# Kernel tuning notes

Hardware: AMD Instinct MI355X
Metric: run time of the kernel (lower is better)

The kernel has to match this reference:

```python
import jax, jax.numpy as jnp
import numpy as np
import math

B, T, C, H = 4, 2048, 1024, 16
EPS = 1e-10

def setup_inputs() -> dict:
    key = jax.random.key(0)
    ks = jax.random.split(key, 9)
    s = 0.02
    return {
        "x": jax.random.normal(ks[0], (B, T, C), jnp.float32),
        "w_attn": jax.random.normal(ks[1], (3 * C, C), jnp.float32) * s,
        "b_attn": jax.random.normal(ks[2], (3 * C,), jnp.float32) * s,
        "w_proj": jax.random.normal(ks[3], (C, C), jnp.float32) * s,
        "b_proj": jax.random.normal(ks[4], (C,), jnp.float32) * s,
        "w_fc": jax.random.normal(ks[5], (4 * C, C), jnp.float32) * s,
        "b_fc": jax.random.normal(ks[6], (4 * C,), jnp.float32) * s,
        "w_mlp_proj": jax.random.normal(ks[7], (C, 4 * C), jnp.float32) * s,
        "b_mlp_proj": jax.random.normal(ks[8], (C,), jnp.float32) * s,
    }

def layernorm(x):
    # custom LayerNormalization: no gamma/beta, eps=1e-10, biased variance
    mean = jnp.mean(x, axis=-1, keepdims=True)
    xmu = x - mean
    var = jnp.mean(xmu * xmu, axis=-1, keepdims=True)
    return xmu / jnp.sqrt(var + EPS)

def new_gelu(x):
    # 0.5*x*(1+tanh(sqrt(2/pi)*(x+0.044715*x^3)))
    c = math.sqrt(2.0 / math.pi)
    return 0.5 * x * (1.0 + jnp.tanh(c * (x + 0.044715 * x * x * x)))

def attention(x, w_attn, b_attn, w_proj, b_proj):
    b, t, cdim = x.shape
    d = cdim // H
    ca = x @ w_attn.T + b_attn                      # [B,T,3C]
    q, k, v = jnp.split(ca, 3, axis=2)
    q = q.reshape(b, t, H, d)
    k = k.reshape(b, t, H, d)
    v = v.reshape(b, t, H, d)
    att = jnp.einsum('bthd,bshd->bhts', q, k) * (1.0 / math.sqrt(d))
    mask = jnp.tril(jnp.ones((t, t), dtype=bool))
    att = jnp.where(mask, att, -jnp.inf)
    att = jax.nn.softmax(att, axis=-1)
    y = jnp.einsum('bhts,bshd->bthd', att, v).reshape(b, t, cdim)
    return y @ w_proj.T + b_proj

def reference(x, w_attn, b_attn, w_proj, b_proj, w_fc, b_fc, w_mlp_proj, b_mlp_proj):
    x = x + attention(layernorm(x), w_attn, b_attn, w_proj, b_proj)
    h = new_gelu(layernorm(x) @ w_fc.T + b_fc)
    x = x + (h @ w_mlp_proj.T + b_mlp_proj)
    return x
```

## Files before the change

kernel.cpp:

```cpp
#include <hip/hip_runtime.h>
#include <math.h>

constexpr int Bb = 4;
constexpr int Tt = 2048;
constexpr int Cc = 1024;
constexpr int Hh = 16;
constexpr int Dh = 64;
constexpr int Mm = Bb * Tt;

typedef __attribute__((ext_vector_type(8))) short s16x8;
typedef __attribute__((ext_vector_type(4))) short s16x4;
typedef __attribute__((ext_vector_type(4))) float f32x4;

__device__ __forceinline__ unsigned short f2bf(float x) {
    unsigned u = __float_as_uint(x);
    u += 0x7FFFu + ((u >> 16) & 1u);
    return (unsigned short)(u >> 16);
}
__device__ __forceinline__ float bf2f(unsigned short h) {
    return __uint_as_float((unsigned)h << 16);
}

__device__ __forceinline__ void gld16(const void* g, void* l) {
    __builtin_amdgcn_global_load_lds(
        (const __attribute__((address_space(1))) void*)g,
        (__attribute__((address_space(3))) void*)l, 16, 0, 0);
}


__global__ __launch_bounds__(256) void ln_conv_kernel(const float* __restrict__ in,
                                                      char* __restrict__ out) {
    const int row = blockIdx.x;
    const float4 v = reinterpret_cast<const float4*>(in + (size_t)row * Cc)[threadIdx.x];
    float s = v.x + v.y + v.z + v.w;
    float q = v.x * v.x + v.y * v.y + v.z * v.z + v.w * v.w;
#pragma unroll
    for (int off = 32; off > 0; off >>= 1) {
        s += __shfl_xor(s, off);
        q += __shfl_xor(q, off);
    }
    __shared__ float red[2][4];
    const int wid = threadIdx.x >> 6;
    if ((threadIdx.x & 63) == 0) { red[0][wid] = s; red[1][wid] = q; }
    __syncthreads();
    s = red[0][0] + red[0][1] + red[0][2] + red[0][3];
    q = red[1][0] + red[1][1] + red[1][2] + red[1][3];
    const float mean = s * (1.0f / Cc);
    const float var = q * (1.0f / Cc) - mean * mean;
    const float rstd = rsqrtf(var + 1e-10f);
    float o[4] = {(v.x - mean) * rstd, (v.y - mean) * rstd,
                  (v.z - mean) * rstd, (v.w - mean) * rstd};
    s16x4 hv, lv;
#pragma unroll
    for (int j = 0; j < 4; ++j) {
        unsigned short h = f2bf(o[j]);
        hv[j] = (short)h;
        lv[j] = (short)f2bf(o[j] - bf2f(h));
    }
    const int c0 = threadIdx.x * 4;
    char* p = out + (size_t)row * 4096 + ((c0 >> 5) * 8 + ((c0 >> 3) & 3)) * 16 + (c0 & 7) * 2;
    *reinterpret_cast<s16x4*>(p) = hv;
    *reinterpret_cast<s16x4*>(p + 64) = lv;
}

__global__ __launch_bounds__(256) void wconv_kernel(const float* __restrict__ W,
                                                    char* __restrict__ out,
                                                    int noct, int oshift, int ldk) {
    const int idx = blockIdx.x * 256 + threadIdx.x;
    if (idx >= noct) return;
    const int r = idx >> oshift;
    const int oct = idx & ((1 << oshift) - 1);
    const float* p = W + (size_t)r * ldk + oct * 8;
    float4 a = *reinterpret_cast<const float4*>(p);
    float4 b = *reinterpret_cast<const float4*>(p + 4);
    float xs[8] = {a.x, a.y, a.z, a.w, b.x, b.y, b.z, b.w};
    s16x8 hv, lv;
#pragma unroll
    for (int j = 0; j < 8; ++j) {
        unsigned short h = f2bf(xs[j]);
        hv[j] = (short)h;
        lv[j] = (short)f2bf(xs[j] - bf2f(h));
    }
    const int Kg = 1 << (oshift - 2);
    char* o = out + (((size_t)r * Kg + (oct >> 2)) * 8 + (oct & 3)) * 16;
    *reinterpret_cast<s16x8*>(o) = hv;
    *reinterpret_cast<s16x8*>(o + 64) = lv;
}

__device__ __forceinline__ float gelu_f(float v) {
    const float z = 1.5957691216057308f * (v + 0.044715f * v * v * v);
    return v / (1.0f + __expf(-z));
}

template <bool GELU, bool RESID, bool CONVOUT, bool ADDBIAS>
__global__ __launch_bounds__(256) void gemm_mfma(
    const char* __restrict__ Ac, const char* __restrict__ Bc,
    const float* __restrict__ bias, const float* __restrict__ resid,
    float* __restrict__ Cout, char* __restrict__ Cconv,
    int M, int N, int K) {
    const int tid = threadIdx.x;
    const int lane = tid & 63;
    const int wid = tid >> 6;
    const int bm = blockIdx.y * 128;
    const int bn = blockIdx.x * 128;
    const int wm = (wid >> 1) * 64;
    const int wn = (wid & 1) * 64;
    const int Kg = K >> 5;

    __shared__ char lds[32768];

    f32x4 acc[4][4];
#pragma unroll
    for (int i = 0; i < 4; ++i)
#pragma unroll
        for (int j = 0; j < 4; ++j) acc[i][j] = (f32x4)0.0f;

    int ur[4], us[4];
#pragma unroll
    for (int i = 0; i < 4; ++i) {
        const int u = tid + i * 256;
        ur[i] = u >> 3;
        us[i] = (u & 7) ^ (ur[i] & 7);
    }

    const int kq = lane >> 4;
    const int fr = lane & 15;

    for (int t = 0; t < Kg; ++t) {
        __syncthreads();
#pragma unroll
        for (int i = 0; i < 4; ++i) {
            const int u = tid + i * 256;
            gld16(Ac + ((((size_t)(bm + ur[i]) * Kg + t) * 8 + us[i]) << 4), lds + u * 16);
            gld16(Bc + ((((size_t)(bn + ur[i]) * Kg + t) * 8 + us[i]) << 4),
                  lds + 16384 + u * 16);
        }
        __syncthreads();

        s16x8 Ah[4], Al[4], Bh[4], Bl[4];
#pragma unroll
        for (int i = 0; i < 4; ++i) {
            const int ra = wm + i * 16 + fr;
            const int pa = kq ^ (ra & 7);
            const char* pA = lds + ra * 128;
            Ah[i] = *reinterpret_cast<const s16x8*>(pA + pa * 16);
            Al[i] = *reinterpret_cast<const s16x8*>(pA + (pa ^ 4) * 16);
            const int rb = wn + i * 16 + fr;
            const int pb = kq ^ (rb & 7);
            const char* pB = lds + 16384 + rb * 128;
            Bh[i] = *reinterpret_cast<const s16x8*>(pB + pb * 16);
            Bl[i] = *reinterpret_cast<const s16x8*>(pB + (pb ^ 4) * 16);
        }
#pragma unroll
        for (int i = 0; i < 4; ++i)
#pragma unroll
            for (int j = 0; j < 4; ++j) {
                acc[i][j] = __builtin_amdgcn_mfma_f32_16x16x32_bf16(Ah[i], Bh[j], acc[i][j], 0, 0, 0);
                acc[i][j] = __builtin_amdgcn_mfma_f32_16x16x32_bf16(Al[i], Bh[j], acc[i][j], 0, 0, 0);
                acc[i][j] = __builtin_amdgcn_mfma_f32_16x16x32_bf16(Ah[i], Bl[j], acc[i][j], 0, 0, 0);
            }
    }

    float bcol[4];
#pragma unroll
    for (int j = 0; j < 4; ++j)
        bcol[j] = ADDBIAS ? bias[bn + wn + j * 16 + fr] : 0.0f;

#pragma unroll
    for (int i = 0; i < 4; ++i) {
#pragma unroll
        for (int rr = 0; rr < 4; ++rr) {
            const int row = bm + wm + i * 16 + ((lane >> 4) << 2) + rr;
#pragma unroll
            for (int j = 0; j < 4; ++j) {
                const int col = bn + wn + j * 16 + fr;
                float v = acc[i][j][rr] + bcol[j];
                if (RESID) v += resid[(size_t)row * N + col];
                if (GELU) v = gelu_f(v);
                if (!CONVOUT) {
                    Cout[(size_t)row * N + col] = v;
                } else {
                    const unsigned short h = f2bf(v);
                    const unsigned short l = f2bf(v - bf2f(h));
                    char* p = Cconv +
                              (((size_t)row * (N >> 5) + (col >> 5)) * 8 + ((col >> 3) & 3)) * 16 +
                              (col & 7) * 2;
                    *reinterpret_cast<unsigned short*>(p) = h;
                    *reinterpret_cast<unsigned short*>(p + 64) = l;
                }
            }
        }
    }
}

__global__ __launch_bounds__(256) void qkv_repack_kernel(
    const float* __restrict__ qkv, unsigned short* __restrict__ qb,
    unsigned short* __restrict__ kb, unsigned short* __restrict__ vtb) {
    const int bh = blockIdx.y;
    const int b = bh >> 4, h = bh & 15;
    const int t0 = blockIdx.x * 64;
    const int tid = threadIdx.x;
    __shared__ unsigned short vtile[64][66];
#pragma unroll
    for (int r = 0; r < 16; ++r) {
        const int idx = tid + r * 256;
        const int t = idx >> 6, d = idx & 63;
        const size_t src = (size_t)(b * Tt + t0 + t) * 3072 + h * 64 + d;
        const size_t dst = ((size_t)bh * Tt + t0 + t) * 64 + d;
        qb[dst] = f2bf(qkv[src] * 0.125f);
        kb[dst] = f2bf(qkv[src + 1024]);
        vtile[t][d] = f2bf(qkv[src + 2048]);
    }
    __syncthreads();
#pragma unroll
    for (int r = 0; r < 16; ++r) {
        const int idx = tid + r * 256;
        const int d = idx >> 6, t = idx & 63;
        vtb[((size_t)bh * 64 + d) * Tt + t0 + t] = vtile[t][d];
    }
}

__global__ __launch_bounds__(256) void attn_mfma_kernel(
    const unsigned short* __restrict__ qbuf, const unsigned short* __restrict__ kbuf,
    const unsigned short* __restrict__ vtbuf, char* __restrict__ yconv) {
    const int qt = blockIdx.x;
    const int bh = blockIdx.y;
    const int tid = threadIdx.x;
    const int w = tid >> 6, lane = tid & 63;
    const int g = lane >> 4, fr = lane & 15;
    const int qbase = qt * 64;

    const unsigned short* Q  = qbuf  + (size_t)bh * Tt * 64;
    const unsigned short* K  = kbuf  + (size_t)bh * Tt * 64;
    const unsigned short* Vt = vtbuf + (size_t)bh * 64 * Tt;

    __shared__ unsigned short Kl[64][72];
    __shared__ unsigned short Vl[64][72];
    __shared__ unsigned short Pl[4][16][72];

    s16x8 qf[2];
#pragma unroll
    for (int s = 0; s < 2; ++s)
        qf[s] = *reinterpret_cast<const s16x8*>(
            &Q[(size_t)(qbase + 16 * w + fr) * 64 + s * 32 + 8 * g]);

    f32x4 acc_o[4];
#pragma unroll
    for (int jd = 0; jd < 4; ++jd) acc_o[jd] = (f32x4)0.0f;
    float lpart[4] = {0.f, 0.f, 0.f, 0.f};

    for (int t0 = 0; t0 <= qt; ++t0) {
        __syncthreads();
#pragma unroll
        for (int r2 = 0; r2 < 2; ++r2) {
            const int idx = tid + r2 * 256;
            const int row = idx >> 3, c = idx & 7;
            *reinterpret_cast<s16x8*>(&Kl[row][c * 8]) =
                *reinterpret_cast<const s16x8*>(&K[(size_t)(t0 * 64 + row) * 64 + c * 8]);
            *reinterpret_cast<s16x8*>(&Vl[row][c * 8]) =
                *reinterpret_cast<const s16x8*>(&Vt[(size_t)row * Tt + t0 * 64 + c * 8]);
        }
        __syncthreads();

        f32x4 acc_s[4];
#pragma unroll
        for (int jk = 0; jk < 4; ++jk) acc_s[jk] = (f32x4)0.0f;
#pragma unroll
        for (int s = 0; s < 2; ++s)
#pragma unroll
            for (int jk = 0; jk < 4; ++jk) {
                const s16x8 kf = *reinterpret_cast<const s16x8*>(
                    &Kl[16 * jk + fr][s * 32 + 8 * g]);
                acc_s[jk] = __builtin_amdgcn_mfma_f32_16x16x32_bf16(qf[s], kf, acc_s[jk], 0, 0, 0);
            }

        const bool diag = (t0 == qt);
#pragma unroll
        for (int jk = 0; jk < 4; ++jk)
#pragma unroll
            for (int rr = 0; rr < 4; ++rr) {
                const int key = 16 * jk + fr;
                const int qrow = 16 * w + 4 * g + rr;
                float p = __expf(acc_s[jk][rr]);
                if (diag && key > qrow) p = 0.0f;
                lpart[rr] += p;
                Pl[w][4 * g + rr][key] = f2bf(p);
            }

#pragma unroll
        for (int s = 0; s < 2; ++s) {
            const s16x8 pf = *reinterpret_cast<const s16x8*>(&Pl[w][fr][s * 32 + 8 * g]);
#pragma unroll
            for (int jd = 0; jd < 4; ++jd) {
                const s16x8 vf = *reinterpret_cast<const s16x8*>(
                    &Vl[16 * jd + fr][s * 32 + 8 * g]);
                acc_o[jd] = __builtin_amdgcn_mfma_f32_16x16x32_bf16(pf, vf, acc_o[jd], 0, 0, 0);
            }
        }
    }

#pragma unroll
    for (int rr = 0; rr < 4; ++rr) {
#pragma unroll
        for (int off = 1; off < 16; off <<= 1)
            lpart[rr] += __shfl_xor(lpart[rr], off);
    }
    float inv[4];
#pragma unroll
    for (int rr = 0; rr < 4; ++rr) inv[rr] = 1.0f / lpart[rr];

    const int bq = bh >> 4;
#pragma unroll
    for (int rr = 0; rr < 4; ++rr) {
        const int row = bq * Tt + qbase + 16 * w + 4 * g + rr;
#pragma unroll
        for (int jd = 0; jd < 4; ++jd) {
            const int col = (bh & 15) * Dh + 16 * jd + fr;
            const float v = acc_o[jd][rr] * inv[rr];
            const unsigned short h = f2bf(v);
            const unsigned short l = f2bf(v - bf2f(h));
            char* p = yconv + (((size_t)row * (Cc >> 5) + (col >> 5)) * 8 + ((col >> 3) & 3)) * 16 +
                      (col & 7) * 2;
            *reinterpret_cast<unsigned short*>(p) = h;
            *reinterpret_cast<unsigned short*>(p + 64) = l;
        }
    }
}

extern "C" void kernel_launch(void* const* d_in, const int* in_sizes, int n_in,
                              void* d_out, int out_size, void* d_ws,
                              size_t ws_size, hipStream_t stream) {
    const float* x      = (const float*)d_in[0];
    const float* w_attn = (const float*)d_in[1];
    const float* b_attn = (const float*)d_in[2];
    const float* w_proj = (const float*)d_in[3];
    const float* b_proj = (const float*)d_in[4];
    const float* w_fc   = (const float*)d_in[5];
    const float* b_fc   = (const float*)d_in[6];
    const float* w_mlp  = (const float*)d_in[7];
    const float* b_mlp  = (const float*)d_in[8];
    float* out = (float*)d_out;

    if (ws_size < (176ull << 20)) return;

    char* ws = (char*)d_ws;
    char*  slotbuf = ws;
    float* qkv     = (float*)(ws + (32ull << 20));
    char*  hconv   = ws + (32ull << 20);
    unsigned short* qb = (unsigned short*)(ws + (128ull << 20));
    unsigned short* kb = (unsigned short*)(ws + (144ull << 20));
    unsigned short* vt = (unsigned short*)(ws + (160ull << 20));
    char*  wscr    = ws + (160ull << 20);
    float* x1      = out;

    ln_conv_kernel<<<Mm, 256, 0, stream>>>(x, slotbuf);
    wconv_kernel<<<1536, 256, 0, stream>>>(w_attn, wscr, 3072 * 128, 7, 1024);
    gemm_mfma<false, false, false, true><<<dim3(24, 64), 256, 0, stream>>>(
        slotbuf, wscr, b_attn, nullptr, qkv, nullptr, Mm, 3 * Cc, Cc);
    qkv_repack_kernel<<<dim3(Tt / 64, Bb * Hh), 256, 0, stream>>>(qkv, qb, kb, vt);
    attn_mfma_kernel<<<dim3(Tt / 64, Bb * Hh), 256, 0, stream>>>(qb, kb, vt, slotbuf);
    wconv_kernel<<<512, 256, 0, stream>>>(w_proj, wscr, 1024 * 128, 7, 1024);
    gemm_mfma<false, true, false, true><<<dim3(8, 64), 256, 0, stream>>>(
        slotbuf, wscr, b_proj, x, x1, nullptr, Mm, Cc, Cc);
    ln_conv_kernel<<<Mm, 256, 0, stream>>>(x1, slotbuf);
    wconv_kernel<<<2048, 256, 0, stream>>>(w_fc, wscr, 4096 * 128, 7, 1024);
    gemm_mfma<true, false, true, true><<<dim3(32, 64), 256, 0, stream>>>(
        slotbuf, wscr, b_fc, nullptr, nullptr, hconv, Mm, 4 * Cc, Cc);
    wconv_kernel<<<2048, 256, 0, stream>>>(w_mlp, wscr, 1024 * 512, 9, 4096);
    gemm_mfma<false, true, false, true><<<dim3(8, 64), 256, 0, stream>>>(
        hconv, wscr, b_mlp, x1, out, nullptr, Mm, Cc, 4 * Cc);
}
```

Measured before the change: 891.4 us.

## Rewrite GEMM as 256x256 tile, 8-wave, double-buffered LDS pipeline with XCD swizzle

Replaces the 128x128 single-buffered MFMA GEMM with a 256x256 tile computed by 8 waves. It double-buffers A/B tiles in 128KB of LDS so the next K-slice loads while the current one is in MFMA. It also remaps workgroup IDs across XCDs for cache locality, uses precomputed 32-bit offsets, and raises wave priority around the MFMA bursts. The costs are much higher LDS use and register pressure. The grids also become smaller (e.g. 128 blocks for the N=1024 GEMMs), which can underfill the 256 CUs.

```diff
diff --git a/kernel.cpp b/kernel.cpp
--- a/kernel.cpp
+++ b/kernel.cpp
@@ -93,7 +93,7 @@
 }
 
 template <bool GELU, bool RESID, bool CONVOUT, bool ADDBIAS>
-__global__ __launch_bounds__(256) void gemm_mfma(
+__global__ __launch_bounds__(512, 2) void gemm_mfma8(
     const char* __restrict__ Ac, const char* __restrict__ Bc,
     const float* __restrict__ bias, const float* __restrict__ resid,
     float* __restrict__ Cout, char* __restrict__ Cconv,
@@ -101,64 +101,99 @@
     const int tid = threadIdx.x;
     const int lane = tid & 63;
     const int wid = tid >> 6;
-    const int bm = blockIdx.y * 128;
-    const int bn = blockIdx.x * 128;
-    const int wm = (wid >> 1) * 64;
-    const int wn = (wid & 1) * 64;
+    const int gx = gridDim.x;
+    const int nwg = gx * gridDim.y;
+    int flat = blockIdx.y * gx + blockIdx.x;
+    flat = (flat & 7) * (nwg >> 3) + (flat >> 3);
+    const int bn = (flat % gx) * 256;
+    const int bm = (flat / gx) * 256;
+    const int wm = (wid >> 2) * 128;
+    const int wn = (wid & 3) * 64;
     const int Kg = K >> 5;
 
-    __shared__ char lds[32768];
-
-    f32x4 acc[4][4];
-#pragma unroll
-    for (int i = 0; i < 4; ++i)
+    __shared__ char lds[131072];
+
+    f32x4 acc[8][4];
+#pragma unroll
+    for (int i = 0; i < 8; ++i)
 #pragma unroll
         for (int j = 0; j < 4; ++j) acc[i][j] = (f32x4)0.0f;
 
-    int ur[4], us[4];
+    unsigned int aoff[4], boff[4], ldso[4];
 #pragma unroll
     for (int i = 0; i < 4; ++i) {
-        const int u = tid + i * 256;
-        ur[i] = u >> 3;
-        us[i] = (u & 7) ^ (ur[i] & 7);
-    }
-
-    const int kq = lane >> 4;
-    const int fr = lane & 15;
-
+        const int u = tid + i * 512;
+        const int r = u >> 3;
+        const int s = (u & 7) ^ (r & 7);
+        aoff[i] = (unsigned int)((bm + r) * Kg * 128 + s * 16);
+        boff[i] = (unsigned int)((bn + r) * Kg * 128 + s * 16);
+        ldso[i] = (unsigned int)(u * 16);
+    }
+
+    const int g = lane >> 4, fr = lane & 15;
+    unsigned int afo[8], bfo[4];
+#pragma unroll
+    for (int i = 0; i < 8; ++i) {
+        const int ra = wm + i * 16 + fr;
+        afo[i] = (unsigned int)(ra * 128 + ((g ^ (ra & 7)) << 4));
+    }
+#pragma unroll
+    for (int j = 0; j < 4; ++j) {
+        const int rb = wn + j * 16 + fr;
+        bfo[j] = (unsigned int)(rb * 128 + ((g ^ (rb & 7)) << 4));
+    }
+
+    auto stage = [&](int tt, int buf) {
+        char* Ad = lds + buf * 65536;
+        char* Bd = Ad + 32768;
+        const unsigned int tb = (unsigned int)tt * 128;
+#pragma unroll
+        for (int i = 0; i < 4; ++i) gld16(Ac + aoff[i] + tb, Ad + ldso[i]);
+#pragma unroll
+        for (int i = 0; i < 4; ++i) gld16(Bc + boff[i] + tb, Bd + ldso[i]);
+    };
+
+    stage(0, 0);
+    asm volatile("s_waitcnt vmcnt(0)" ::: "memory");
+    __builtin_amdgcn_s_barrier();
+
+    s16x8 Bh[4], Bl[4];
     for (int t = 0; t < Kg; ++t) {
-        __syncthreads();
-#pragma unroll
-        for (int i = 0; i < 4; ++i) {
-            const int u = tid + i * 256;
-            gld16(Ac + ((((size_t)(bm + ur[i]) * Kg + t) * 8 + us[i]) << 4), lds + u * 16);
-            gld16(Bc + ((((size_t)(bn + ur[i]) * Kg + t) * 8 + us[i]) << 4),
-                  lds + 16384 + u * 16);
+        const int c = t & 1;
+        const char* Ab = lds + c * 65536;
+        const char* Bb = Ab + 32768;
+#pragma unroll
+        for (int q = 0; q < 4; ++q) {
+            if (q == 0) {
+#pragma unroll
+                for (int j = 0; j < 4; ++j) {
+                    Bh[j] = *reinterpret_cast<const s16x8*>(Bb + bfo[j]);
+                    Bl[j] = *reinterpret_cast<const s16x8*>(Bb + (bfo[j] ^ 64u));
+                }
+            }
+            const s16x8 Ah0 = *reinterpret_cast<const s16x8*>(Ab + afo[2 * q]);
+            const s16x8 Al0 = *reinterpret_cast<const s16x8*>(Ab + (afo[2 * q] ^ 64u));
+            const s16x8 Ah1 = *reinterpret_cast<const s16x8*>(Ab + afo[2 * q + 1]);
+            const s16x8 Al1 = *reinterpret_cast<const s16x8*>(Ab + (afo[2 * q + 1] ^ 64u));
+            if (q == 0 && t + 1 < Kg) stage(t + 1, c ^ 1);
+            __builtin_amdgcn_s_barrier();
+            asm volatile("s_waitcnt lgkmcnt(0)" ::: "memory");
+            __builtin_amdgcn_sched_barrier(0);
+            __builtin_amdgcn_s_setprio(1);
+#pragma unroll
+            for (int j = 0; j < 4; ++j) {
+                acc[2 * q][j] = __builtin_amdgcn_mfma_f32_16x16x32_bf16(Ah0, Bh[j], acc[2 * q][j], 0, 0, 0);
+                acc[2 * q][j] = __builtin_amdgcn_mfma_f32_16x16x32_bf16(Al0, Bh[j], acc[2 * q][j], 0, 0, 0);
+                acc[2 * q][j] = __builtin_amdgcn_mfma_f32_16x16x32_bf16(Ah0, Bl[j], acc[2 * q][j], 0, 0, 0);
+                acc[2 * q + 1][j] = __builtin_amdgcn_mfma_f32_16x16x32_bf16(Ah1, Bh[j], acc[2 * q + 1][j], 0, 0, 0);
+                acc[2 * q + 1][j] = __builtin_amdgcn_mfma_f32_16x16x32_bf16(Al1, Bh[j], acc[2 * q + 1][j], 0, 0, 0);
+                acc[2 * q + 1][j] = __builtin_amdgcn_mfma_f32_16x16x32_bf16(Ah1, Bl[j], acc[2 * q + 1][j], 0, 0, 0);
+            }
+            __builtin_amdgcn_s_setprio(0);
+            __builtin_amdgcn_sched_barrier(0);
+            if (q == 3) asm volatile("s_waitcnt vmcnt(0)" ::: "memory");
+            __builtin_amdgcn_s_barrier();
         }
-        __syncthreads();
-
-        s16x8 Ah[4], Al[4], Bh[4], Bl[4];
-#pragma unroll
-        for (int i = 0; i < 4; ++i) {
-            const int ra = wm + i * 16 + fr;
-            const int pa = kq ^ (ra & 7);
-            const char* pA = lds + ra * 128;
-            Ah[i] = *reinterpret_cast<const s16x8*>(pA + pa * 16);
-            Al[i] = *reinterpret_cast<const s16x8*>(pA + (pa ^ 4) * 16);
-            const int rb = wn + i * 16 + fr;
-            const int pb = kq ^ (rb & 7);
-            const char* pB = lds + 16384 + rb * 128;
-            Bh[i] = *reinterpret_cast<const s16x8*>(pB + pb * 16);
-            Bl[i] = *reinterpret_cast<const s16x8*>(pB + (pb ^ 4) * 16);
-        }
-#pragma unroll
-        for (int i = 0; i < 4; ++i)
-#pragma unroll
-            for (int j = 0; j < 4; ++j) {
-                acc[i][j] = __builtin_amdgcn_mfma_f32_16x16x32_bf16(Ah[i], Bh[j], acc[i][j], 0, 0, 0);
-                acc[i][j] = __builtin_amdgcn_mfma_f32_16x16x32_bf16(Al[i], Bh[j], acc[i][j], 0, 0, 0);
-                acc[i][j] = __builtin_amdgcn_mfma_f32_16x16x32_bf16(Ah[i], Bl[j], acc[i][j], 0, 0, 0);
-            }
     }
 
     float bcol[4];
@@ -167,10 +202,10 @@
         bcol[j] = ADDBIAS ? bias[bn + wn + j * 16 + fr] : 0.0f;
 
 #pragma unroll
-    for (int i = 0; i < 4; ++i) {
+    for (int i = 0; i < 8; ++i) {
 #pragma unroll
         for (int rr = 0; rr < 4; ++rr) {
-            const int row = bm + wm + i * 16 + ((lane >> 4) << 2) + rr;
+            const int row = bm + wm + i * 16 + g * 4 + rr;
 #pragma unroll
             for (int j = 0; j < 4; ++j) {
                 const int col = bn + wn + j * 16 + fr;
@@ -355,18 +390,18 @@
 
     ln_conv_kernel<<<Mm, 256, 0, stream>>>(x, slotbuf);
     wconv_kernel<<<1536, 256, 0, stream>>>(w_attn, wscr, 3072 * 128, 7, 1024);
-    gemm_mfma<false, false, false, true><<<dim3(24, 64), 256, 0, stream>>>(
+    gemm_mfma8<false, false, false, true><<<dim3(12, 32), 512, 0, stream>>>(
         slotbuf, wscr, b_attn, nullptr, qkv, nullptr, Mm, 3 * Cc, Cc);
     qkv_repack_kernel<<<dim3(Tt / 64, Bb * Hh), 256, 0, stream>>>(qkv, qb, kb, vt);
     attn_mfma_kernel<<<dim3(Tt / 64, Bb * Hh), 256, 0, stream>>>(qb, kb, vt, slotbuf);
     wconv_kernel<<<512, 256, 0, stream>>>(w_proj, wscr, 1024 * 128, 7, 1024);
-    gemm_mfma<false, true, false, true><<<dim3(8, 64), 256, 0, stream>>>(
+    gemm_mfma8<false, true, false, true><<<dim3(4, 32), 512, 0, stream>>>(
         slotbuf, wscr, b_proj, x, x1, nullptr, Mm, Cc, Cc);
     ln_conv_kernel<<<Mm, 256, 0, stream>>>(x1, slotbuf);
     wconv_kernel<<<2048, 256, 0, stream>>>(w_fc, wscr, 4096 * 128, 7, 1024);
-    gemm_mfma<true, false, true, true><<<dim3(32, 64), 256, 0, stream>>>(
+    gemm_mfma8<true, false, true, true><<<dim3(16, 32), 512, 0, stream>>>(
         slotbuf, wscr, b_fc, nullptr, nullptr, hconv, Mm, 4 * Cc, Cc);
     wconv_kernel<<<2048, 256, 0, stream>>>(w_mlp, wscr, 1024 * 512, 9, 4096);
-    gemm_mfma<false, true, false, true><<<dim3(8, 64), 256, 0, stream>>>(
+    gemm_mfma8<false, true, false, true><<<dim3(4, 32), 512, 0, stream>>>(
         hconv, wscr, b_mlp, x1, out, nullptr, Mm, Cc, 4 * Cc);
 }
```

Measured after the change: 996.9 us. +11.8%, slower.
